# Performance work log

Hardware: AMD Instinct MI355X
Metric: run time of the kernel (lower is better)

## Reference

```python
import jax, jax.numpy as jnp
import numpy as np

N_PER_DEG = 30000
MAX_DEG = 6
MIN_DEG = 0
N_ATOMS = N_PER_DEG * (MAX_DEG + 1)  # 210000, atoms sorted by degree
N_FEAT = 128
NB_FILTER = 128
NB_AFFINE = 2 * MAX_DEG + (1 - MIN_DEG)  # 13


def setup_inputs() -> dict:
    key = jax.random.key(0)
    ks = jax.random.split(key, 2 + MAX_DEG)
    atoms = jax.random.normal(ks[0], (N_ATOMS, N_FEAT), dtype=jnp.float32)
    # glorot-ish scale for the 13 affine weights
    W = jax.random.normal(ks[1], (NB_AFFINE, N_FEAT, NB_FILTER), dtype=jnp.float32) * (1.0 / np.sqrt(N_FEAT))
    b = jnp.zeros((NB_AFFINE, NB_FILTER), dtype=jnp.float32)
    # deg_slice[d] = (start, count) for degree d in 0..MAX_DEG; equal-size buckets
    deg_slice = jnp.asarray(
        np.stack([np.arange(MAX_DEG + 1) * N_PER_DEG,
                  np.full(MAX_DEG + 1, N_PER_DEG)], axis=1).astype(np.int32))
    inp = {"atoms": atoms, "W": W, "b": b, "deg_slice": deg_slice}
    for d in range(1, MAX_DEG + 1):
        inp[f"adj{d}"] = jax.random.randint(ks[1 + d], (N_PER_DEG, d), 0, N_ATOMS, dtype=jnp.int32)
    return inp


def reference(atoms, W, b, deg_slice, adj1, adj2, adj3, adj4, adj5, adj6):
    """Degree-bucketed graph convolution (deepchem GraphConv, linear activation).

    W ordering matches the original iterator: for deg=1..MAX_DEG the pair
    (rel=W[2*(deg-1)], self=W[2*(deg-1)+1]), then deg-0 self uses W[2*MAX_DEG].
    Output concat order: deg 0 bucket first, then deg 1..MAX_DEG.
    """
    adjs = [adj1, adj2, adj3, adj4, adj5, adj6]
    ds = np.asarray(deg_slice)  # structural constant: static slice bounds
    outs = [None] * (MAX_DEG + 1 - MIN_DEG)
    # deg 0: self-affine only
    s0, c0 = int(ds[0, 0]), int(ds[0, 1])
    outs[0] = atoms[s0:s0 + c0] @ W[2 * MAX_DEG] + b[2 * MAX_DEG]
    for deg in range(1, MAX_DEG + 1):
        s, c = int(ds[deg, 0]), int(ds[deg, 1])
        # gather neighbors of each degree-deg atom and sum: (c, deg, F) -> (c, F)
        rel = jnp.take(atoms, adjs[deg - 1], axis=0).sum(axis=1)
        out = (rel @ W[2 * (deg - 1)] + b[2 * (deg - 1)]
               + atoms[s:s + c] @ W[2 * (deg - 1) + 1] + b[2 * (deg - 1) + 1])
        outs[deg] = out
    return jnp.concatenate(outs, axis=0)  # (N_ATOMS, NB_FILTER)
```

## Files before the change

kernel.cpp:

```cpp
#include <hip/hip_runtime.h>
#include <hip/hip_bf16.h>

#define NPD 30000
#define NF  128
#define MAXDEG 6
#define TM  64
#define LDK 136

typedef __attribute__((ext_vector_type(8))) short short8;
typedef __attribute__((ext_vector_type(4))) float floatx4;

__device__ __forceinline__ unsigned short f2bf(float f) {
    __hip_bfloat16 h = __float2bfloat16(f);
    return __builtin_bit_cast(unsigned short, h);
}
__device__ __forceinline__ float bf2f(unsigned short u) {
    unsigned v = ((unsigned)u) << 16; return __builtin_bit_cast(float, v);
}
__device__ __forceinline__ uint4 pack16B(float4 a, float4 b) {
    uint4 v;
    v.x = (unsigned)f2bf(a.x) | ((unsigned)f2bf(a.y) << 16);
    v.y = (unsigned)f2bf(a.z) | ((unsigned)f2bf(a.w) << 16);
    v.z = (unsigned)f2bf(b.x) | ((unsigned)f2bf(b.y) << 16);
    v.w = (unsigned)f2bf(b.z) | ((unsigned)f2bf(b.w) << 16);
    return v;
}
__device__ __forceinline__ void addu4(float* s, uint4 h) {
    s[0] += bf2f((unsigned short)h.x); s[1] += bf2f((unsigned short)(h.x >> 16));
    s[2] += bf2f((unsigned short)h.y); s[3] += bf2f((unsigned short)(h.y >> 16));
    s[4] += bf2f((unsigned short)h.z); s[5] += bf2f((unsigned short)(h.z >> 16));
    s[6] += bf2f((unsigned short)h.w); s[7] += bf2f((unsigned short)(h.w >> 16));
}

__global__ void wt_kernel(const float* __restrict__ W,
                          unsigned short* __restrict__ Wt) {
    __shared__ unsigned short t[32][33];
    const int a  = blockIdx.z;
    const int k0 = blockIdx.x * 32, n0 = blockIdx.y * 32;
    const int tx = threadIdx.x & 31, ty = threadIdx.x >> 5;
    const float*    Wp  = W  + (size_t)a * NF * NF;
    unsigned short* Wtp = Wt + (size_t)a * NF * NF;
#pragma unroll
    for (int i = 0; i < 32; i += 8)
        t[ty + i][tx] = f2bf(Wp[(size_t)(k0 + ty + i) * NF + (n0 + tx)]);
    __syncthreads();
#pragma unroll
    for (int i = 0; i < 32; i += 8)
        Wtp[(size_t)(n0 + ty + i) * NF + (k0 + tx)] = t[tx][ty + i];
}

__global__ __launch_bounds__(256) void cvt_kernel(const float* __restrict__ src,
                                                  unsigned short* __restrict__ dst) {
    const size_t i = (size_t)blockIdx.x * 256 + threadIdx.x;
    const size_t n8 = (size_t)NPD * (MAXDEG + 1) * NF / 8;
    if (i < n8) {
        const float4* p = (const float4*)(src + i * 8);
        ((uint4*)dst)[i] = pack16B(p[0], p[1]);
    }
}

__device__ __forceinline__ void load_bfr(short8 b[4], const float* __restrict__ Wf,
                                         const unsigned short* __restrict__ Wt,
                                         int use_wt, int wi, int kk,
                                         int col0, int nb, int kq) {
    if (use_wt) {
        const unsigned short* Wp = Wt + (size_t)wi * NF * NF;
#pragma unroll
        for (int nt = 0; nt < 4; ++nt)
            b[nt] = *(const short8*)(Wp + (size_t)(col0 + nt * 16 + nb) * NF + kk * 32 + kq);
    } else {
        const float* Wp = Wf + (size_t)wi * NF * NF;
#pragma unroll
        for (int nt = 0; nt < 4; ++nt) {
            short8 f;
#pragma unroll
            for (int j = 0; j < 8; ++j)
                f[j] = (short)f2bf(Wp[(size_t)(kk * 32 + kq + j) * NF + col0 + nt * 16 + nb]);
            b[nt] = f;
        }
    }
}

template <int DEG, bool BF16A>
__device__ __forceinline__ void degree_work(
    const float* __restrict__ atomsF, const unsigned short* __restrict__ atomsH,
    const float* __restrict__ W, const unsigned short* __restrict__ Wt,
    const float* __restrict__ bvec, const int* __restrict__ adj,
    int use_wt, float* __restrict__ out,
    unsigned short* sA, int* sIdx)
{
    const int tid  = threadIdx.x;
    const int lane = tid & 63, wave = tid >> 6;
    const int wr = wave >> 1, wc = wave & 1;
    const int row0_local = blockIdx.x * TM;
    const int valid = min(TM, NPD - row0_local);
    const int row0g = DEG * NPD + row0_local;
    const int nb = lane & 15;
    const int kq = (lane >> 4) * 8;
    const int col0 = wc * 64;
    const int wi_self = (DEG == 0) ? 12 : (2 * DEG - 1);
    const int wi_rel  = (DEG > 0) ? 2 * (DEG - 1) : 0;

    floatx4 acc[2][4];
#pragma unroll
    for (int i = 0; i < 2; i++)
#pragma unroll
        for (int j = 0; j < 4; j++) acc[i][j] = (floatx4){0.f, 0.f, 0.f, 0.f};

    if (DEG > 0) {
        for (int i = tid; i < valid * DEG; i += 256)
            sIdx[i] = adj[(size_t)row0_local * DEG + i];
    }

#pragma unroll
    for (int p = 0; p < 4; ++p) {
        int idx = p * 256 + tid;
        int r = idx >> 4, ch = (idx & 15) * 8;
        int rr = min(r, valid - 1);
        uint4 v;
        if (BF16A) {
            v = *(const uint4*)(atomsH + (size_t)(row0g + rr) * NF + ch);
        } else {
            const float4* pf = (const float4*)(atomsF + (size_t)(row0g + rr) * NF + ch);
            v = pack16B(pf[0], pf[1]);
        }
        *(uint4*)&sA[r * LDK + ch] = v;
    }
    __syncthreads();

    auto run_phase = [&](int wi) {
#pragma unroll
        for (int kk = 0; kk < 4; ++kk) {
            short8 bfr[4];
            load_bfr(bfr, W, Wt, use_wt, wi, kk, col0, nb, kq);
            short8 af[2];
#pragma unroll
            for (int mt = 0; mt < 2; ++mt)
                af[mt] = *(const short8*)&sA[(wr * 32 + mt * 16 + nb) * LDK + kk * 32 + kq];
#pragma unroll
            for (int mt = 0; mt < 2; ++mt)
#pragma unroll
                for (int nt = 0; nt < 4; ++nt)
                    acc[mt][nt] = __builtin_amdgcn_mfma_f32_16x16x32_bf16(
                        af[mt], bfr[nt], acc[mt][nt], 0, 0, 0);
        }
    };

    run_phase(wi_self);

    if constexpr (DEG > 0) {
        __syncthreads();
#pragma unroll
        for (int p = 0; p < 2; ++p) {
            int idx = p * 256 + tid;
            int r = idx >> 3, kc = (idx & 7) * 16;
            int rr = min(r, valid - 1);
            int idxs[DEG];
#pragma unroll
            for (int j = 0; j < DEG; ++j) idxs[j] = sIdx[rr * DEG + j];
            float s[16];
#pragma unroll
            for (int i = 0; i < 16; ++i) s[i] = 0.f;
#pragma unroll
            for (int j = 0; j < DEG; ++j) {
                if (BF16A) {
                    const uint4* ph = (const uint4*)(atomsH + (size_t)idxs[j] * NF + kc);
                    uint4 h0 = ph[0], h1 = ph[1];
                    addu4(s, h0); addu4(s + 8, h1);
                } else {
                    const float4* pf = (const float4*)(atomsF + (size_t)idxs[j] * NF + kc);
                    float4 q0 = pf[0], q1 = pf[1], q2 = pf[2], q3 = pf[3];
                    s[0]  += q0.x; s[1]  += q0.y; s[2]  += q0.z; s[3]  += q0.w;
                    s[4]  += q1.x; s[5]  += q1.y; s[6]  += q1.z; s[7]  += q1.w;
                    s[8]  += q2.x; s[9]  += q2.y; s[10] += q2.z; s[11] += q2.w;
                    s[12] += q3.x; s[13] += q3.y; s[14] += q3.z; s[15] += q3.w;
                }
            }
            uint4 w0, w1;
            w0.x = (unsigned)f2bf(s[0])  | ((unsigned)f2bf(s[1])  << 16);
            w0.y = (unsigned)f2bf(s[2])  | ((unsigned)f2bf(s[3])  << 16);
            w0.z = (unsigned)f2bf(s[4])  | ((unsigned)f2bf(s[5])  << 16);
            w0.w = (unsigned)f2bf(s[6])  | ((unsigned)f2bf(s[7])  << 16);
            w1.x = (unsigned)f2bf(s[8])  | ((unsigned)f2bf(s[9])  << 16);
            w1.y = (unsigned)f2bf(s[10]) | ((unsigned)f2bf(s[11]) << 16);
            w1.z = (unsigned)f2bf(s[12]) | ((unsigned)f2bf(s[13]) << 16);
            w1.w = (unsigned)f2bf(s[14]) | ((unsigned)f2bf(s[15]) << 16);
            *(uint4*)&sA[r * LDK + kc]     = w0;
            *(uint4*)&sA[r * LDK + kc + 8] = w1;
        }
        __syncthreads();
        run_phase(wi_rel);
    }

    float bias[4];
#pragma unroll
    for (int nt = 0; nt < 4; ++nt) {
        const int n = col0 + nt * 16 + nb;
        float bv = bvec[wi_self * NF + n];
        if (DEG > 0) bv += bvec[wi_rel * NF + n];
        bias[nt] = bv;
    }
    const int rq = (lane >> 4) * 4;
#pragma unroll
    for (int mt = 0; mt < 2; ++mt) {
#pragma unroll
        for (int reg = 0; reg < 4; ++reg) {
            const int r = wr * 32 + mt * 16 + rq + reg;
            if (r < valid) {
                float* op = out + (size_t)(row0g + r) * NF;
#pragma unroll
                for (int nt = 0; nt < 4; ++nt)
                    op[col0 + nt * 16 + nb] = acc[mt][nt][reg] + bias[nt];
            }
        }
    }
}

template <bool BF16A>
__global__ __launch_bounds__(256) void gconv_kernel(
    const float* __restrict__ atomsF, const unsigned short* __restrict__ atomsH,
    const float* __restrict__ W, const unsigned short* __restrict__ Wt,
    const float* __restrict__ bvec,
    const int* __restrict__ adj1, const int* __restrict__ adj2,
    const int* __restrict__ adj3, const int* __restrict__ adj4,
    const int* __restrict__ adj5, const int* __restrict__ adj6,
    const int use_wt, float* __restrict__ out)
{
    __shared__ unsigned short sA[TM * LDK];
    __shared__ int sIdx[TM * MAXDEG];
    switch (blockIdx.y) {
        case 0: degree_work<0, BF16A>(atomsF, atomsH, W, Wt, bvec, nullptr, use_wt, out, sA, sIdx); break;
        case 1: degree_work<1, BF16A>(atomsF, atomsH, W, Wt, bvec, adj1,    use_wt, out, sA, sIdx); break;
        case 2: degree_work<2, BF16A>(atomsF, atomsH, W, Wt, bvec, adj2,    use_wt, out, sA, sIdx); break;
        case 3: degree_work<3, BF16A>(atomsF, atomsH, W, Wt, bvec, adj3,    use_wt, out, sA, sIdx); break;
        case 4: degree_work<4, BF16A>(atomsF, atomsH, W, Wt, bvec, adj4,    use_wt, out, sA, sIdx); break;
        case 5: degree_work<5, BF16A>(atomsF, atomsH, W, Wt, bvec, adj5,    use_wt, out, sA, sIdx); break;
        default: degree_work<6, BF16A>(atomsF, atomsH, W, Wt, bvec, adj6,   use_wt, out, sA, sIdx); break;
    }
}

extern "C" void kernel_launch(void* const* d_in, const int* in_sizes, int n_in,
                              void* d_out, int out_size, void* d_ws, size_t ws_size,
                              hipStream_t stream) {
    const float* atoms = (const float*)d_in[0];
    const float* W     = (const float*)d_in[1];
    const float* b     = (const float*)d_in[2];
    const int* adj1 = (const int*)d_in[4];
    const int* adj2 = (const int*)d_in[5];
    const int* adj3 = (const int*)d_in[6];
    const int* adj4 = (const int*)d_in[7];
    const int* adj5 = (const int*)d_in[8];
    const int* adj6 = (const int*)d_in[9];

    const size_t wt_bytes = (size_t)13 * NF * NF * sizeof(unsigned short);
    const size_t at_bytes = (size_t)NPD * (MAXDEG + 1) * NF * sizeof(unsigned short);
    const int use_wt   = (ws_size >= wt_bytes) ? 1 : 0;
    const int use_bf16 = (ws_size >= wt_bytes + at_bytes) ? 1 : 0;
    unsigned short* Wt     = (unsigned short*)d_ws;
    unsigned short* atomsH = (unsigned short*)((char*)d_ws + wt_bytes);

    if (use_wt)
        wt_kernel<<<dim3(4, 4, 13), 256, 0, stream>>>(W, Wt);
    if (use_bf16) {
        const int n8 = NPD * (MAXDEG + 1) * NF / 8;
        cvt_kernel<<<(n8 + 255) / 256, 256, 0, stream>>>(atoms, atomsH);
        gconv_kernel<true><<<dim3((NPD + TM - 1) / TM, MAXDEG + 1), 256, 0, stream>>>(
            atoms, atomsH, W, Wt, b, adj1, adj2, adj3, adj4, adj5, adj6, use_wt,
            (float*)d_out);
    } else {
        gconv_kernel<false><<<dim3((NPD + TM - 1) / TM, MAXDEG + 1), 256, 0, stream>>>(
            atoms, atomsH, W, Wt, b, adj1, adj2, adj3, adj4, adj5, adj6, use_wt,
            (float*)d_out);
    }
}
```

Baseline: 272.3 us.

## Split into gather kernel and fused self+rel GEMM kernel with concatenated K

Replaces the three-kernel pipeline (weight transpose, full atoms bf16 conversion, fused gather+GEMM) with two kernels. A gather kernel sums neighbor rows in fp32 and writes bf16 rel sums to a workspace, with weight transposition folded in as extra blocks. A GEMM kernel then runs one K=256 MFMA pass over concatenated self and rel tiles using 32-row tiles. This drops the full atoms bf16 conversion pass and the mid-kernel barrier between phases. In exchange it writes and rereads a rel buffer, gathers fp32 rows, uses smaller tiles, and falls back to a slow naive kernel when the workspace is too small.

```diff
diff --git a/kernel.cpp b/kernel.cpp
--- a/kernel.cpp
+++ b/kernel.cpp
@@ -4,8 +4,7 @@
 #define NPD 30000
 #define NF  128
 #define MAXDEG 6
-#define TM  64
-#define LDK 136
+#define LDK2 264
 
 typedef __attribute__((ext_vector_type(8))) short short8;
 typedef __attribute__((ext_vector_type(4))) float floatx4;
@@ -13,9 +12,6 @@
 __device__ __forceinline__ unsigned short f2bf(float f) {
     __hip_bfloat16 h = __float2bfloat16(f);
     return __builtin_bit_cast(unsigned short, h);
-}
-__device__ __forceinline__ float bf2f(unsigned short u) {
-    unsigned v = ((unsigned)u) << 16; return __builtin_bit_cast(float, v);
 }
 __device__ __forceinline__ uint4 pack16B(float4 a, float4 b) {
     uint4 v;
@@ -25,18 +21,12 @@
     v.w = (unsigned)f2bf(b.z) | ((unsigned)f2bf(b.w) << 16);
     return v;
 }
-__device__ __forceinline__ void addu4(float* s, uint4 h) {
-    s[0] += bf2f((unsigned short)h.x); s[1] += bf2f((unsigned short)(h.x >> 16));
-    s[2] += bf2f((unsigned short)h.y); s[3] += bf2f((unsigned short)(h.y >> 16));
-    s[4] += bf2f((unsigned short)h.z); s[5] += bf2f((unsigned short)(h.z >> 16));
-    s[6] += bf2f((unsigned short)h.w); s[7] += bf2f((unsigned short)(h.w >> 16));
-}
-
-__global__ void wt_kernel(const float* __restrict__ W,
-                          unsigned short* __restrict__ Wt) {
-    __shared__ unsigned short t[32][33];
-    const int a  = blockIdx.z;
-    const int k0 = blockIdx.x * 32, n0 = blockIdx.y * 32;
+
+__device__ __forceinline__ void wt_tile(const float* __restrict__ W,
+                                        unsigned short* __restrict__ Wt,
+                                        int bx, unsigned short (*t)[33]) {
+    const int a  = bx >> 4;
+    const int k0 = ((bx >> 2) & 3) * 32, n0 = (bx & 3) * 32;
     const int tx = threadIdx.x & 31, ty = threadIdx.x >> 5;
     const float*    Wp  = W  + (size_t)a * NF * NF;
     unsigned short* Wtp = Wt + (size_t)a * NF * NF;
@@ -49,152 +39,130 @@
         Wtp[(size_t)(n0 + ty + i) * NF + (k0 + tx)] = t[tx][ty + i];
 }
 
-__global__ __launch_bounds__(256) void cvt_kernel(const float* __restrict__ src,
-                                                  unsigned short* __restrict__ dst) {
-    const size_t i = (size_t)blockIdx.x * 256 + threadIdx.x;
-    const size_t n8 = (size_t)NPD * (MAXDEG + 1) * NF / 8;
-    if (i < n8) {
-        const float4* p = (const float4*)(src + i * 8);
-        ((uint4*)dst)[i] = pack16B(p[0], p[1]);
-    }
-}
-
-__device__ __forceinline__ void load_bfr(short8 b[4], const float* __restrict__ Wf,
-                                         const unsigned short* __restrict__ Wt,
-                                         int use_wt, int wi, int kk,
-                                         int col0, int nb, int kq) {
-    if (use_wt) {
-        const unsigned short* Wp = Wt + (size_t)wi * NF * NF;
-#pragma unroll
-        for (int nt = 0; nt < 4; ++nt)
-            b[nt] = *(const short8*)(Wp + (size_t)(col0 + nt * 16 + nb) * NF + kk * 32 + kq);
-    } else {
-        const float* Wp = Wf + (size_t)wi * NF * NF;
-#pragma unroll
-        for (int nt = 0; nt < 4; ++nt) {
-            short8 f;
-#pragma unroll
-            for (int j = 0; j < 8; ++j)
-                f[j] = (short)f2bf(Wp[(size_t)(kk * 32 + kq + j) * NF + col0 + nt * 16 + nb]);
-            b[nt] = f;
-        }
-    }
-}
-
-template <int DEG, bool BF16A>
-__device__ __forceinline__ void degree_work(
-    const float* __restrict__ atomsF, const unsigned short* __restrict__ atomsH,
-    const float* __restrict__ W, const unsigned short* __restrict__ Wt,
-    const float* __restrict__ bvec, const int* __restrict__ adj,
-    int use_wt, float* __restrict__ out,
-    unsigned short* sA, int* sIdx)
+template <int DEG>
+__device__ __forceinline__ void gather_work(const float* __restrict__ atoms,
+                                            const int* __restrict__ adj,
+                                            unsigned short* __restrict__ relbuf) {
+    const int t = threadIdx.x;
+    const int r = blockIdx.x * 32 + (t >> 3);
+    if (r >= NPD) return;
+    const int c = (t & 7) * 16;
+    const int* arow = adj + (size_t)r * DEG;
+    int idxs[DEG];
+#pragma unroll
+    for (int j = 0; j < DEG; ++j) idxs[j] = arow[j];
+    float s[16];
+#pragma unroll
+    for (int i = 0; i < 16; ++i) s[i] = 0.f;
+#pragma unroll
+    for (int j = 0; j < DEG; ++j) {
+        const float4* p = (const float4*)(atoms + (size_t)idxs[j] * NF + c);
+        float4 q0 = p[0], q1 = p[1], q2 = p[2], q3 = p[3];
+        s[0]  += q0.x; s[1]  += q0.y; s[2]  += q0.z; s[3]  += q0.w;
+        s[4]  += q1.x; s[5]  += q1.y; s[6]  += q1.z; s[7]  += q1.w;
+        s[8]  += q2.x; s[9]  += q2.y; s[10] += q2.z; s[11] += q2.w;
+        s[12] += q3.x; s[13] += q3.y; s[14] += q3.z; s[15] += q3.w;
+    }
+    uint4 w0 = pack16B(make_float4(s[0], s[1], s[2], s[3]),
+                       make_float4(s[4], s[5], s[6], s[7]));
+    uint4 w1 = pack16B(make_float4(s[8], s[9], s[10], s[11]),
+                       make_float4(s[12], s[13], s[14], s[15]));
+    unsigned short* op = relbuf + ((size_t)(DEG - 1) * NPD + r) * NF + c;
+    *(uint4*)op       = w0;
+    *(uint4*)(op + 8) = w1;
+}
+
+__global__ __launch_bounds__(256) void gather_kernel(
+    const float* __restrict__ atoms, const float* __restrict__ W,
+    unsigned short* __restrict__ Wt,
+    const int* __restrict__ adj1, const int* __restrict__ adj2,
+    const int* __restrict__ adj3, const int* __restrict__ adj4,
+    const int* __restrict__ adj5, const int* __restrict__ adj6,
+    unsigned short* __restrict__ relbuf)
+{
+    __shared__ unsigned short t[32][33];
+    if (blockIdx.y == 6) {
+        if (blockIdx.x < 208) wt_tile(W, Wt, blockIdx.x, t);
+        return;
+    }
+    switch (blockIdx.y) {
+        case 0: gather_work<1>(atoms, adj1, relbuf); break;
+        case 1: gather_work<2>(atoms, adj2, relbuf); break;
+        case 2: gather_work<3>(atoms, adj3, relbuf); break;
+        case 3: gather_work<4>(atoms, adj4, relbuf); break;
+        case 4: gather_work<5>(atoms, adj5, relbuf); break;
+        default: gather_work<6>(atoms, adj6, relbuf); break;
+    }
+}
+
+template <int DEG>
+__device__ __forceinline__ void gemm_work(
+    const float* __restrict__ atomsF, const unsigned short* __restrict__ relbuf,
+    const unsigned short* __restrict__ Wt, const float* __restrict__ bvec,
+    float* __restrict__ out, unsigned short* __restrict__ sA)
 {
     const int tid  = threadIdx.x;
     const int lane = tid & 63, wave = tid >> 6;
-    const int wr = wave >> 1, wc = wave & 1;
-    const int row0_local = blockIdx.x * TM;
-    const int valid = min(TM, NPD - row0_local);
-    const int row0g = DEG * NPD + row0_local;
     const int nb = lane & 15;
     const int kq = (lane >> 4) * 8;
-    const int col0 = wc * 64;
+    const int col0 = wave * 32;
+    const int row0_local = blockIdx.x * 32;
+    const int valid = min(32, NPD - row0_local);
+    const int row0g = DEG * NPD + row0_local;
     const int wi_self = (DEG == 0) ? 12 : (2 * DEG - 1);
     const int wi_rel  = (DEG > 0) ? 2 * (DEG - 1) : 0;
 
-    floatx4 acc[2][4];
+    floatx4 acc[2][2];
 #pragma unroll
     for (int i = 0; i < 2; i++)
 #pragma unroll
-        for (int j = 0; j < 4; j++) acc[i][j] = (floatx4){0.f, 0.f, 0.f, 0.f};
-
-    if (DEG > 0) {
-        for (int i = tid; i < valid * DEG; i += 256)
-            sIdx[i] = adj[(size_t)row0_local * DEG + i];
-    }
-
-#pragma unroll
-    for (int p = 0; p < 4; ++p) {
+        for (int j = 0; j < 2; j++) acc[i][j] = (floatx4){0.f, 0.f, 0.f, 0.f};
+
+#pragma unroll
+    for (int p = 0; p < 2; ++p) {
         int idx = p * 256 + tid;
         int r = idx >> 4, ch = (idx & 15) * 8;
         int rr = min(r, valid - 1);
-        uint4 v;
-        if (BF16A) {
-            v = *(const uint4*)(atomsH + (size_t)(row0g + rr) * NF + ch);
-        } else {
-            const float4* pf = (const float4*)(atomsF + (size_t)(row0g + rr) * NF + ch);
-            v = pack16B(pf[0], pf[1]);
-        }
-        *(uint4*)&sA[r * LDK + ch] = v;
-    }
-    __syncthreads();
-
-    auto run_phase = [&](int wi) {
-#pragma unroll
-        for (int kk = 0; kk < 4; ++kk) {
-            short8 bfr[4];
-            load_bfr(bfr, W, Wt, use_wt, wi, kk, col0, nb, kq);
-            short8 af[2];
-#pragma unroll
-            for (int mt = 0; mt < 2; ++mt)
-                af[mt] = *(const short8*)&sA[(wr * 32 + mt * 16 + nb) * LDK + kk * 32 + kq];
-#pragma unroll
-            for (int mt = 0; mt < 2; ++mt)
-#pragma unroll
-                for (int nt = 0; nt < 4; ++nt)
-                    acc[mt][nt] = __builtin_amdgcn_mfma_f32_16x16x32_bf16(
-                        af[mt], bfr[nt], acc[mt][nt], 0, 0, 0);
-        }
-    };
-
-    run_phase(wi_self);
-
+        const float4* pf = (const float4*)(atomsF + (size_t)(row0g + rr) * NF + ch);
+        *(uint4*)&sA[r * LDK2 + ch] = pack16B(pf[0], pf[1]);
+    }
     if constexpr (DEG > 0) {
-        __syncthreads();
 #pragma unroll
         for (int p = 0; p < 2; ++p) {
             int idx = p * 256 + tid;
-            int r = idx >> 3, kc = (idx & 7) * 16;
+            int r = idx >> 4, ch = (idx & 15) * 8;
             int rr = min(r, valid - 1);
-            int idxs[DEG];
-#pragma unroll
-            for (int j = 0; j < DEG; ++j) idxs[j] = sIdx[rr * DEG + j];
-            float s[16];
-#pragma unroll
-            for (int i = 0; i < 16; ++i) s[i] = 0.f;
-#pragma unroll
-            for (int j = 0; j < DEG; ++j) {
-                if (BF16A) {
-                    const uint4* ph = (const uint4*)(atomsH + (size_t)idxs[j] * NF + kc);
-                    uint4 h0 = ph[0], h1 = ph[1];
-                    addu4(s, h0); addu4(s + 8, h1);
-                } else {
-                    const float4* pf = (const float4*)(atomsF + (size_t)idxs[j] * NF + kc);
-                    float4 q0 = pf[0], q1 = pf[1], q2 = pf[2], q3 = pf[3];
-                    s[0]  += q0.x; s[1]  += q0.y; s[2]  += q0.z; s[3]  += q0.w;
-                    s[4]  += q1.x; s[5]  += q1.y; s[6]  += q1.z; s[7]  += q1.w;
-                    s[8]  += q2.x; s[9]  += q2.y; s[10] += q2.z; s[11] += q2.w;
-                    s[12] += q3.x; s[13] += q3.y; s[14] += q3.z; s[15] += q3.w;
-                }
-            }
-            uint4 w0, w1;
-            w0.x = (unsigned)f2bf(s[0])  | ((unsigned)f2bf(s[1])  << 16);
-            w0.y = (unsigned)f2bf(s[2])  | ((unsigned)f2bf(s[3])  << 16);
-            w0.z = (unsigned)f2bf(s[4])  | ((unsigned)f2bf(s[5])  << 16);
-            w0.w = (unsigned)f2bf(s[6])  | ((unsigned)f2bf(s[7])  << 16);
-            w1.x = (unsigned)f2bf(s[8])  | ((unsigned)f2bf(s[9])  << 16);
-            w1.y = (unsigned)f2bf(s[10]) | ((unsigned)f2bf(s[11]) << 16);
-            w1.z = (unsigned)f2bf(s[12]) | ((unsigned)f2bf(s[13]) << 16);
-            w1.w = (unsigned)f2bf(s[14]) | ((unsigned)f2bf(s[15]) << 16);
-            *(uint4*)&sA[r * LDK + kc]     = w0;
-            *(uint4*)&sA[r * LDK + kc + 8] = w1;
+            *(uint4*)&sA[r * LDK2 + NF + ch] =
+                *(const uint4*)(relbuf + ((size_t)(DEG - 1) * NPD + row0_local + rr) * NF + ch);
         }
-        __syncthreads();
-        run_phase(wi_rel);
-    }
-
-    float bias[4];
-#pragma unroll
-    for (int nt = 0; nt < 4; ++nt) {
+    }
+    __syncthreads();
+
+    constexpr int NKK = (DEG > 0) ? 8 : 4;
+#pragma unroll
+    for (int kk = 0; kk < NKK; ++kk) {
+        const int wi = (kk < 4) ? wi_self : wi_rel;
+        const unsigned short* Wp = Wt + (size_t)wi * NF * NF;
+        short8 bfr[2];
+#pragma unroll
+        for (int nt = 0; nt < 2; ++nt)
+            bfr[nt] = *(const short8*)(Wp + (size_t)(col0 + nt * 16 + nb) * NF
+                                          + (kk & 3) * 32 + kq);
+        short8 af[2];
+#pragma unroll
+        for (int mt = 0; mt < 2; ++mt)
+            af[mt] = *(const short8*)&sA[(mt * 16 + nb) * LDK2 + kk * 32 + kq];
+#pragma unroll
+        for (int mt = 0; mt < 2; ++mt)
+#pragma unroll
+            for (int nt = 0; nt < 2; ++nt)
+                acc[mt][nt] = __builtin_amdgcn_mfma_f32_16x16x32_bf16(
+                    af[mt], bfr[nt], acc[mt][nt], 0, 0, 0);
+    }
+
+    float bias[2];
+#pragma unroll
+    for (int nt = 0; nt < 2; ++nt) {
         const int n = col0 + nt * 16 + nb;
         float bv = bvec[wi_self * NF + n];
         if (DEG > 0) bv += bvec[wi_rel * NF + n];
@@ -205,38 +173,63 @@
     for (int mt = 0; mt < 2; ++mt) {
 #pragma unroll
         for (int reg = 0; reg < 4; ++reg) {
-            const int r = wr * 32 + mt * 16 + rq + reg;
+            const int r = mt * 16 + rq + reg;
             if (r < valid) {
                 float* op = out + (size_t)(row0g + r) * NF;
 #pragma unroll
-                for (int nt = 0; nt < 4; ++nt)
+                for (int nt = 0; nt < 2; ++nt)
                     op[col0 + nt * 16 + nb] = acc[mt][nt][reg] + bias[nt];
             }
         }
     }
 }
 
-template <bool BF16A>
-__global__ __launch_bounds__(256) void gconv_kernel(
-    const float* __restrict__ atomsF, const unsigned short* __restrict__ atomsH,
-    const float* __restrict__ W, const unsigned short* __restrict__ Wt,
-    const float* __restrict__ bvec,
+__global__ __launch_bounds__(256) void gemm_kernel(
+    const float* __restrict__ atomsF, const unsigned short* __restrict__ relbuf,
+    const unsigned short* __restrict__ Wt, const float* __restrict__ bvec,
+    float* __restrict__ out)
+{
+    __shared__ unsigned short sA[32 * LDK2];
+    switch (blockIdx.y) {
+        case 0: gemm_work<0>(atomsF, relbuf, Wt, bvec, out, sA); break;
+        case 1: gemm_work<1>(atomsF, relbuf, Wt, bvec, out, sA); break;
+        case 2: gemm_work<2>(atomsF, relbuf, Wt, bvec, out, sA); break;
+        case 3: gemm_work<3>(atomsF, relbuf, Wt, bvec, out, sA); break;
+        case 4: gemm_work<4>(atomsF, relbuf, Wt, bvec, out, sA); break;
+        case 5: gemm_work<5>(atomsF, relbuf, Wt, bvec, out, sA); break;
+        default: gemm_work<6>(atomsF, relbuf, Wt, bvec, out, sA); break;
+    }
+}
+
+__global__ __launch_bounds__(128) void naive_kernel(
+    const float* __restrict__ atoms, const float* __restrict__ W,
+    const float* __restrict__ b,
     const int* __restrict__ adj1, const int* __restrict__ adj2,
     const int* __restrict__ adj3, const int* __restrict__ adj4,
     const int* __restrict__ adj5, const int* __restrict__ adj6,
-    const int use_wt, float* __restrict__ out)
-{
-    __shared__ unsigned short sA[TM * LDK];
-    __shared__ int sIdx[TM * MAXDEG];
-    switch (blockIdx.y) {
-        case 0: degree_work<0, BF16A>(atomsF, atomsH, W, Wt, bvec, nullptr, use_wt, out, sA, sIdx); break;
-        case 1: degree_work<1, BF16A>(atomsF, atomsH, W, Wt, bvec, adj1,    use_wt, out, sA, sIdx); break;
-        case 2: degree_work<2, BF16A>(atomsF, atomsH, W, Wt, bvec, adj2,    use_wt, out, sA, sIdx); break;
-        case 3: degree_work<3, BF16A>(atomsF, atomsH, W, Wt, bvec, adj3,    use_wt, out, sA, sIdx); break;
-        case 4: degree_work<4, BF16A>(atomsF, atomsH, W, Wt, bvec, adj4,    use_wt, out, sA, sIdx); break;
-        case 5: degree_work<5, BF16A>(atomsF, atomsH, W, Wt, bvec, adj5,    use_wt, out, sA, sIdx); break;
-        default: degree_work<6, BF16A>(atomsF, atomsH, W, Wt, bvec, adj6,   use_wt, out, sA, sIdx); break;
-    }
+    float* __restrict__ out)
+{
+    const int i = blockIdx.x;
+    const int deg = i / NPD, r = i - deg * NPD, n = threadIdx.x;
+    __shared__ float selfr[NF], relr[NF];
+    selfr[n] = atoms[(size_t)i * NF + n];
+    float rv = 0.f;
+    if (deg > 0) {
+        const int* adjs[6] = {adj1, adj2, adj3, adj4, adj5, adj6};
+        const int* adj = adjs[deg - 1];
+        for (int j = 0; j < deg; ++j)
+            rv += atoms[(size_t)adj[(size_t)r * deg + j] * NF + n];
+    }
+    relr[n] = rv;
+    __syncthreads();
+    const int ws  = (deg == 0) ? 12 : 2 * deg - 1;
+    const int wrl = 2 * (deg - 1);
+    float acc = b[ws * NF + n] + ((deg > 0) ? b[wrl * NF + n] : 0.f);
+    for (int k = 0; k < NF; ++k) {
+        acc += selfr[k] * W[(size_t)ws * NF * NF + (size_t)k * NF + n];
+        if (deg > 0) acc += relr[k] * W[(size_t)wrl * NF * NF + (size_t)k * NF + n];
+    }
+    out[(size_t)i * NF + n] = acc;
 }
 
 extern "C" void kernel_launch(void* const* d_in, const int* in_sizes, int n_in,
@@ -252,24 +245,19 @@
     const int* adj5 = (const int*)d_in[8];
     const int* adj6 = (const int*)d_in[9];
 
-    const size_t wt_bytes = (size_t)13 * NF * NF * sizeof(unsigned short);
-    const size_t at_bytes = (size_t)NPD * (MAXDEG + 1) * NF * sizeof(unsigned short);
-    const int use_wt   = (ws_size >= wt_bytes) ? 1 : 0;
-    const int use_bf16 = (ws_size >= wt_bytes + at_bytes) ? 1 : 0;
-    unsigned short* Wt     = (unsigned short*)d_ws;
-    unsigned short* atomsH = (unsigned short*)((char*)d_ws + wt_bytes);
-
-    if (use_wt)
-        wt_kernel<<<dim3(4, 4, 13), 256, 0, stream>>>(W, Wt);
-    if (use_bf16) {
-        const int n8 = NPD * (MAXDEG + 1) * NF / 8;
-        cvt_kernel<<<(n8 + 255) / 256, 256, 0, stream>>>(atoms, atomsH);
-        gconv_kernel<true><<<dim3((NPD + TM - 1) / TM, MAXDEG + 1), 256, 0, stream>>>(
-            atoms, atomsH, W, Wt, b, adj1, adj2, adj3, adj4, adj5, adj6, use_wt,
-            (float*)d_out);
+    const size_t wt_bytes  = (size_t)13 * NF * NF * sizeof(unsigned short);
+    const size_t rel_bytes = (size_t)6 * NPD * NF * sizeof(unsigned short);
+
+    if (ws_size >= wt_bytes + rel_bytes) {
+        unsigned short* Wt     = (unsigned short*)d_ws;
+        unsigned short* relbuf = (unsigned short*)((char*)d_ws + wt_bytes);
+        const int gx = (NPD + 31) / 32;
+        gather_kernel<<<dim3(gx, 7), 256, 0, stream>>>(
+            atoms, W, Wt, adj1, adj2, adj3, adj4, adj5, adj6, relbuf);
+        gemm_kernel<<<dim3(gx, 7), 256, 0, stream>>>(atoms, relbuf, Wt, b,
+                                                     (float*)d_out);
     } else {
-        gconv_kernel<false><<<dim3((NPD + TM - 1) / TM, MAXDEG + 1), 256, 0, stream>>>(
-            atoms, atomsH, W, Wt, b, adj1, adj2, adj3, adj4, adj5, adj6, use_wt,
-            (float*)d_out);
-    }
-}
+        naive_kernel<<<NPD * (MAXDEG + 1), NF, 0, stream>>>(
+            atoms, W, b, adj1, adj2, adj3, adj4, adj5, adj6, (float*)d_out);
+    }
+}
```

After: 299.5 us. 1.1x slower.
